# Optimization experiments

Hardware: AMD Instinct MI355X
Metric: run time of the kernel (lower is better)

Reference implementation:

```python
import jax, jax.numpy as jnp
import numpy as np

WINDOW = 128  # causal window width
D_SCALE = None  # set from val dim at trace time


def _softsign(x):
    return x / (1.0 + jnp.abs(x))


def setup_inputs() -> dict:
    key = jax.random.key(0)
    k1, k2 = jax.random.split(key)
    B, N, D = 4, 4096, 256
    val = jax.random.normal(k1, (B, N, D), dtype=jnp.float32)
    state = jax.random.normal(k2, (B, N), dtype=jnp.float32)
    return {"val": val, "state": state}


def reference(val, state):
    # val: [B, N, D], state: [B, N]
    B, N, D = val.shape
    # pairwise_fn: scaled dot product -> scores [B, N, N]
    scores = jnp.einsum('bnd,bmd->bnm', val, val) / jnp.sqrt(jnp.asarray(D, val.dtype))
    # edge_compress_fn: softsign
    edges = _softsign(scores)
    # causal window mask: source j satisfies (j <= i) & (j >= i - window)
    i = jnp.arange(N)[:, None]
    j = jnp.arange(N)[None, :]
    mask = (j <= i) & (j >= i - WINDOW)  # [N, N]
    edges = edges * mask[None, :, :].astype(edges.dtype)
    # val_proj_fn / state_proj_fn are Identity
    delta_state = jnp.einsum('bij,bj->bi', edges, state)   # [B, N]
    delta_val = jnp.einsum('bij,bjd->bid', edges, val)      # [B, N, D]
    return (delta_state, delta_val)
```

## Files before the change

### kernel.cpp

```cpp
#include <hip/hip_runtime.h>

#define NSEQ 4096
#define DIM  256
#define WIN  128
#define BATCH 4

typedef __bf16 bf16x8 __attribute__((ext_vector_type(8)));
typedef float  f32x4  __attribute__((ext_vector_type(4)));
typedef int    v2i    __attribute__((ext_vector_type(2)));
typedef int    v4i    __attribute__((ext_vector_type(4)));

__device__ __forceinline__ int sub_off(int j, int d) {
    return (((j >> 2) * 16 + (d >> 4)) << 6) + ((j & 3) << 4) + (d & 15);
}

__device__ __forceinline__ unsigned short f2bf(float f) {
    unsigned u = __builtin_bit_cast(unsigned, f);
    u += 0x7fffu + ((u >> 16) & 1u);
    return (unsigned short)(u >> 16);
}

__global__ __launch_bounds__(256, 2)
void sp_kernel(const float* __restrict__ val,
               const float* __restrict__ state,
               float* __restrict__ out) {
    __shared__ __align__(128) unsigned short vbuf[3][8192];
    __shared__ __align__(128) unsigned short E_s[2][32 * 56];
    __shared__ float ds_part[4][16];

    const int bx  = blockIdx.x;
    const int lbx = ((bx & 7) << 6) + (bx >> 3);
    const int b      = lbx >> 7;
    const int tile_i = lbx & 127;
    const int r0     = tile_i << 5;

    const int t   = threadIdx.x;
    const int w   = t >> 6;
    const int l   = t & 63;
    const int l15 = l & 15;
    const int l4  = l >> 4;
    const int mt  = w >> 1;
    const int jt  = w & 1;

    const float* valb = val + ((size_t)b * NSEQ) * DIM;
    const float* stb  = state + ((size_t)b * NSEQ);
    float* out_state  = out + ((size_t)b * NSEQ);
    float* out_val    = out + (size_t)BATCH * NSEQ + ((size_t)b * NSEQ) * DIM;

    const int s_jl[2] = {(w << 2) + l4, (w << 2) + l4 + 16};

    {
        const float* src = valb + ((size_t)tile_i << 13);
        #pragma unroll
        for (int p = 0; p < 8; ++p) {
            const int jl = s_jl[p & 1];
            const int d0 = (l15 << 2) + ((p >> 1) << 6);
            float4 v = *reinterpret_cast<const float4*>(src + jl * DIM + d0);
            ushort4 hh;
            hh.x = f2bf(v.x); hh.y = f2bf(v.y); hh.z = f2bf(v.z); hh.w = f2bf(v.w);
            *reinterpret_cast<ushort4*>(&vbuf[0][sub_off(jl, d0)]) = hh;
        }
    }
    __syncthreads();

    const int il = (mt << 4) + l15;
    const int jl = (jt << 4) + l15;
    bf16x8 af[8], sb[8];
    #pragma unroll
    for (int ks = 0; ks < 8; ++ks) {
        af[ks] = *reinterpret_cast<const bf16x8*>(&vbuf[0][sub_off(il, (l4 << 3) + (ks << 5))]);
        sb[ks] = *reinterpret_cast<const bf16x8*>(&vbuf[0][sub_off(jl, (l4 << 3) + (ks << 5))]);
    }

    const int tj0   = (tile_i >= 4) ? (tile_i - 4) : 0;
    const int ntile = tile_i - tj0 + 1;

    float dsacc[4] = {0.f, 0.f, 0.f, 0.f};
    f32x4 accpv[2][4];
    #pragma unroll
    for (int m2 = 0; m2 < 2; ++m2)
        #pragma unroll
        for (int tt = 0; tt < 4; ++tt)
            accpv[m2][tt] = (f32x4){0.f, 0.f, 0.f, 0.f};

    int bpi = 0;
    for (int q = 0; q < ntile; ++q) {
        const int ti = tile_i - q;
        const bool havenext = (q + 1 < ntile);
        const int bni = (bpi == 2) ? 0 : bpi + 1;
        const unsigned short* bp = &vbuf[bpi][0];
        unsigned short* bn = &vbuf[bni][0];
        unsigned short* Ecur = &E_s[q & 1][0];

        const int jg = (ti << 5) + jl;
        const float stv = stb[jg];
        float4 stg[8];
        if (havenext) {
            const float* src = valb + ((size_t)(ti - 1) << 13);
            #pragma unroll
            for (int qq = 0; qq < 8; ++qq)
                stg[qq] = *reinterpret_cast<const float4*>(src + s_jl[qq & 1] * DIM
                                                           + (l15 << 2) + ((qq >> 1) << 6));
        }

        f32x4 acc = (f32x4){0.f, 0.f, 0.f, 0.f};
        __builtin_amdgcn_s_setprio(1);
        #pragma unroll
        for (int ks = 0; ks < 8; ++ks)
            acc = __builtin_amdgcn_mfma_f32_16x16x32_bf16(af[ks], sb[ks], acc, 0, 0, 0);
        __builtin_amdgcn_s_setprio(0);

        const int ib = r0 + (mt << 4) + (l4 << 2);
        #pragma unroll
        for (int r = 0; r < 4; ++r) {
            float s = acc[r] * 0.0625f;
            float e = s / (1.0f + fabsf(s));
            const int ig = ib + r;
            if (jg > ig || jg < ig - WIN) e = 0.0f;
            dsacc[r] += e * stv;
            Ecur[((mt << 4) + (l4 << 2) + r) * 56 + (jt << 4) + l15] = f2bf(e);
        }

        if (havenext) {
            #pragma unroll
            for (int qq = 0; qq < 8; ++qq) {
                ushort4 hh;
                hh.x = f2bf(stg[qq].x); hh.y = f2bf(stg[qq].y);
                hh.z = f2bf(stg[qq].z); hh.w = f2bf(stg[qq].w);
                *reinterpret_cast<ushort4*>(&bn[sub_off(s_jl[qq & 1],
                                                        (l15 << 2) + ((qq >> 1) << 6))]) = hh;
            }
        }
        __syncthreads();

        bf16x8 ef0 = *reinterpret_cast<const bf16x8*>(&Ecur[l15 * 56 + (l4 << 3)]);
        bf16x8 ef1 = *reinterpret_cast<const bf16x8*>(&Ecur[(16 + l15) * 56 + (l4 << 3)]);
        if (havenext) {
            #pragma unroll
            for (int ks = 0; ks < 8; ++ks)
                sb[ks] = *reinterpret_cast<const bf16x8*>(&bn[sub_off(jl, (l4 << 3) + (ks << 5))]);
        }
        const unsigned lds_base = (unsigned)(size_t)bp;
        v2i tr[8];
        #pragma unroll
        for (int tt = 0; tt < 4; ++tt) {
            const int nt = (w << 2) + tt;
            unsigned a0 = lds_base + (unsigned)((((l4 << 5) + nt) << 7) + (l15 << 3));
            asm volatile("ds_read_b64_tr_b16 %0, %1" : "=v"(tr[2 * tt]) : "v"(a0) : "memory");
            asm volatile("ds_read_b64_tr_b16 %0, %1 offset:2048" : "=v"(tr[2 * tt + 1]) : "v"(a0) : "memory");
        }
        asm volatile("s_waitcnt lgkmcnt(0)" ::: "memory");
        __builtin_amdgcn_sched_barrier(0);
        __builtin_amdgcn_s_setprio(1);
        #pragma unroll
        for (int tt = 0; tt < 4; ++tt) {
            v4i tmp;
            tmp.x = tr[2 * tt].x; tmp.y = tr[2 * tt].y;
            tmp.z = tr[2 * tt + 1].x; tmp.w = tr[2 * tt + 1].y;
            bf16x8 bfr = __builtin_bit_cast(bf16x8, tmp);
            accpv[0][tt] = __builtin_amdgcn_mfma_f32_16x16x32_bf16(ef0, bfr, accpv[0][tt], 0, 0, 0);
            accpv[1][tt] = __builtin_amdgcn_mfma_f32_16x16x32_bf16(ef1, bfr, accpv[1][tt], 0, 0, 0);
        }
        __builtin_amdgcn_s_setprio(0);
        bpi = bni;
    }

    #pragma unroll
    for (int m = 1; m <= 8; m <<= 1) {
        #pragma unroll
        for (int r = 0; r < 4; ++r)
            dsacc[r] += __shfl_xor(dsacc[r], m, 64);
    }
    if (l15 == 0) {
        #pragma unroll
        for (int r = 0; r < 4; ++r)
            ds_part[w][(l4 << 2) + r] = dsacc[r];
    }
    __syncthreads();
    if (t < 32) {
        const int m2 = t >> 4;
        out_state[r0 + t] = ds_part[(m2 << 1)][t & 15] + ds_part[(m2 << 1) + 1][t & 15];
    }

    #pragma unroll
    for (int m2 = 0; m2 < 2; ++m2) {
        #pragma unroll
        for (int tt = 0; tt < 4; ++tt) {
            const int d = (w << 6) + (tt << 4) + l15;
            #pragma unroll
            for (int r = 0; r < 4; ++r) {
                const int ig = r0 + (m2 << 4) + (l4 << 2) + r;
                out_val[(size_t)ig * DIM + d] = accpv[m2][tt][r];
            }
        }
    }
}

extern "C" void kernel_launch(void* const* d_in, const int* in_sizes, int n_in,
                              void* d_out, int out_size, void* d_ws, size_t ws_size,
                              hipStream_t stream) {
    const float* val   = (const float*)d_in[0];
    const float* state = (const float*)d_in[1];
    float* out = (float*)d_out;
    sp_kernel<<<dim3(BATCH * (NSEQ / 32)), dim3(256), 0, stream>>>(val, state, out);
}
```

Measured before the change: 17.20 us.

## Prefetch global tiles two iterations ahead with packed bf16 conversion

Global loads of the val tiles now run two iterations ahead of use, alternating between two register staging arrays, and the first prefetch is issued alongside the initial tile load. The loop is fully unrolled to five iterations so buffer indices become compile-time constants. The float-to-bf16 conversion for staging uses the packed v_cvt_pk_bf16_f32 instruction, and the softsign divide is replaced by a hardware reciprocal. The aim is to hide global memory latency behind the MFMA work and cut conversion and divide ALU cost, in exchange for roughly 32 more VGPRs under a 2-waves-per-SIMD launch bound, which may cause spills.

Measured after the change: 16.98 us. About the same (-1.3%).

```diff
diff --git a/kernel.cpp b/kernel.cpp
--- a/kernel.cpp
+++ b/kernel.cpp
@@ -18,6 +18,34 @@
     unsigned u = __builtin_bit_cast(unsigned, f);
     u += 0x7fffu + ((u >> 16) & 1u);
     return (unsigned short)(u >> 16);
+}
+
+__device__ __forceinline__ unsigned pk2bf(float lo, float hi) {
+    unsigned r;
+    asm("v_cvt_pk_bf16_f32 %0, %1, %2" : "=v"(r) : "v"(lo), "v"(hi));
+    return r;
+}
+
+__device__ __forceinline__ void issue_loads(const float* __restrict__ src,
+                                            const int s_jl0, const int s_jl1,
+                                            const int l15, float4 (&dst)[8]) {
+    #pragma unroll
+    for (int qq = 0; qq < 8; ++qq)
+        dst[qq] = *reinterpret_cast<const float4*>(src + (qq & 1 ? s_jl1 : s_jl0) * DIM
+                                                   + (l15 << 2) + ((qq >> 1) << 6));
+}
+
+__device__ __forceinline__ void stage_write(unsigned short* __restrict__ bn,
+                                            const int s_jl0, const int s_jl1,
+                                            const int l15, const float4 (&stg)[8]) {
+    #pragma unroll
+    for (int qq = 0; qq < 8; ++qq) {
+        uint2 u;
+        u.x = pk2bf(stg[qq].x, stg[qq].y);
+        u.y = pk2bf(stg[qq].z, stg[qq].w);
+        *reinterpret_cast<uint2*>(&bn[sub_off(qq & 1 ? s_jl1 : s_jl0,
+                                              (l15 << 2) + ((qq >> 1) << 6))]) = u;
+    }
 }
 
 __global__ __launch_bounds__(256, 2)
@@ -47,19 +75,20 @@
     float* out_state  = out + ((size_t)b * NSEQ);
     float* out_val    = out + (size_t)BATCH * NSEQ + ((size_t)b * NSEQ) * DIM;
 
-    const int s_jl[2] = {(w << 2) + l4, (w << 2) + l4 + 16};
+    const int s_jl0 = (w << 2) + l4;
+    const int s_jl1 = s_jl0 + 16;
+
+    const int tj0   = (tile_i >= 4) ? (tile_i - 4) : 0;
+    const int ntile = tile_i - tj0 + 1;
+
+    float4 stgA[8], stgB[8];
 
     {
-        const float* src = valb + ((size_t)tile_i << 13);
-        #pragma unroll
-        for (int p = 0; p < 8; ++p) {
-            const int jl = s_jl[p & 1];
-            const int d0 = (l15 << 2) + ((p >> 1) << 6);
-            float4 v = *reinterpret_cast<const float4*>(src + jl * DIM + d0);
-            ushort4 hh;
-            hh.x = f2bf(v.x); hh.y = f2bf(v.y); hh.z = f2bf(v.z); hh.w = f2bf(v.w);
-            *reinterpret_cast<ushort4*>(&vbuf[0][sub_off(jl, d0)]) = hh;
-        }
+        float4 pv[8];
+        issue_loads(valb + ((size_t)tile_i << 13), s_jl0, s_jl1, l15, pv);
+        if (ntile > 1)
+            issue_loads(valb + ((size_t)(tile_i - 1) << 13), s_jl0, s_jl1, l15, stgB);
+        stage_write(&vbuf[0][0], s_jl0, s_jl1, l15, pv);
     }
     __syncthreads();
 
@@ -72,9 +101,6 @@
         sb[ks] = *reinterpret_cast<const bf16x8*>(&vbuf[0][sub_off(jl, (l4 << 3) + (ks << 5))]);
     }
 
-    const int tj0   = (tile_i >= 4) ? (tile_i - 4) : 0;
-    const int ntile = tile_i - tj0 + 1;
-
     float dsacc[4] = {0.f, 0.f, 0.f, 0.f};
     f32x4 accpv[2][4];
     #pragma unroll
@@ -83,24 +109,24 @@
         for (int tt = 0; tt < 4; ++tt)
             accpv[m2][tt] = (f32x4){0.f, 0.f, 0.f, 0.f};
 
-    int bpi = 0;
-    for (int q = 0; q < ntile; ++q) {
-        const int ti = tile_i - q;
-        const bool havenext = (q + 1 < ntile);
-        const int bni = (bpi == 2) ? 0 : bpi + 1;
-        const unsigned short* bp = &vbuf[bpi][0];
-        unsigned short* bn = &vbuf[bni][0];
+    #pragma unroll
+    for (int q = 0; q < 5; ++q) {
+        if (q >= ntile) break;
+        const int ti  = tile_i - q;
+        const int cs  = q % 3;
+        const int ns  = (q + 1) % 3;
+        const unsigned short* bp = &vbuf[cs][0];
+        unsigned short* bn = &vbuf[ns][0];
         unsigned short* Ecur = &E_s[q & 1][0];
 
         const int jg = (ti << 5) + jl;
         const float stv = stb[jg];
-        float4 stg[8];
-        if (havenext) {
-            const float* src = valb + ((size_t)(ti - 1) << 13);
-            #pragma unroll
-            for (int qq = 0; qq < 8; ++qq)
-                stg[qq] = *reinterpret_cast<const float4*>(src + s_jl[qq & 1] * DIM
-                                                           + (l15 << 2) + ((qq >> 1) << 6));
+
+        if (q + 2 < ntile) {
+            if ((q & 1) == 0)
+                issue_loads(valb + ((size_t)(ti - 2) << 13), s_jl0, s_jl1, l15, stgA);
+            else
+                issue_loads(valb + ((size_t)(ti - 2) << 13), s_jl0, s_jl1, l15, stgB);
         }
 
         f32x4 acc = (f32x4){0.f, 0.f, 0.f, 0.f};
@@ -114,28 +140,24 @@
         #pragma unroll
         for (int r = 0; r < 4; ++r) {
             float s = acc[r] * 0.0625f;
-            float e = s / (1.0f + fabsf(s));
+            float e = s * __builtin_amdgcn_rcpf(1.0f + fabsf(s));
             const int ig = ib + r;
             if (jg > ig || jg < ig - WIN) e = 0.0f;
             dsacc[r] += e * stv;
             Ecur[((mt << 4) + (l4 << 2) + r) * 56 + (jt << 4) + l15] = f2bf(e);
         }
 
-        if (havenext) {
-            #pragma unroll
-            for (int qq = 0; qq < 8; ++qq) {
-                ushort4 hh;
-                hh.x = f2bf(stg[qq].x); hh.y = f2bf(stg[qq].y);
-                hh.z = f2bf(stg[qq].z); hh.w = f2bf(stg[qq].w);
-                *reinterpret_cast<ushort4*>(&bn[sub_off(s_jl[qq & 1],
-                                                        (l15 << 2) + ((qq >> 1) << 6))]) = hh;
-            }
+        if (q + 1 < ntile) {
+            if ((q & 1) == 0)
+                stage_write(bn, s_jl0, s_jl1, l15, stgB);
+            else
+                stage_write(bn, s_jl0, s_jl1, l15, stgA);
         }
         __syncthreads();
 
         bf16x8 ef0 = *reinterpret_cast<const bf16x8*>(&Ecur[l15 * 56 + (l4 << 3)]);
         bf16x8 ef1 = *reinterpret_cast<const bf16x8*>(&Ecur[(16 + l15) * 56 + (l4 << 3)]);
-        if (havenext) {
+        if (q + 1 < ntile) {
             #pragma unroll
             for (int ks = 0; ks < 8; ++ks)
                 sb[ks] = *reinterpret_cast<const bf16x8*>(&bn[sub_off(jl, (l4 << 3) + (ks << 5))]);
@@ -155,14 +177,13 @@
         #pragma unroll
         for (int tt = 0; tt < 4; ++tt) {
             v4i tmp;
-            tmp.x = tr[2 * tt].x; tmp.y = tr[2 * tt].y;
+            tmp.x = tr[2 * tt].x;     tmp.y = tr[2 * tt].y;
             tmp.z = tr[2 * tt + 1].x; tmp.w = tr[2 * tt + 1].y;
             bf16x8 bfr = __builtin_bit_cast(bf16x8, tmp);
             accpv[0][tt] = __builtin_amdgcn_mfma_f32_16x16x32_bf16(ef0, bfr, accpv[0][tt], 0, 0, 0);
             accpv[1][tt] = __builtin_amdgcn_mfma_f32_16x16x32_bf16(ef1, bfr, accpv[1][tt], 0, 0, 0);
         }
         __builtin_amdgcn_s_setprio(0);
-        bpi = bni;
     }
 
     #pragma unroll
```

## Shrink LDS to double buffers and raise occupancy to four blocks per CU

Applied to the files above, without the earlier changes.

Cuts the val staging buffers from three to two and the edge buffer from two to one, and adds a second barrier per iteration so the buffers can be reused safely. Lowers LDS use and register pressure (sb is now loaded just before the QK MFMAs instead of prefetched) so launch bounds can ask for four blocks per CU. Also swaps the manual bf16 rounding for the packed v_cvt_pk_bf16_f32 instruction and the softsign division for a fast reciprocal. The extra barrier and the loss of the sb prefetch add per-iteration latency in exchange for more waves to hide it.

After: 47.44 us. 2.76x slower.

```diff
diff --git a/kernel.cpp b/kernel.cpp
--- a/kernel.cpp
+++ b/kernel.cpp
@@ -20,12 +20,18 @@
     return (unsigned short)(u >> 16);
 }
 
-__global__ __launch_bounds__(256, 2)
+__device__ __forceinline__ unsigned pk2bf(float lo, float hi) {
+    unsigned r;
+    asm("v_cvt_pk_bf16_f32 %0, %1, %2" : "=v"(r) : "v"(lo), "v"(hi));
+    return r;
+}
+
+__global__ __launch_bounds__(256, 4)
 void sp_kernel(const float* __restrict__ val,
                const float* __restrict__ state,
                float* __restrict__ out) {
-    __shared__ __align__(128) unsigned short vbuf[3][8192];
-    __shared__ __align__(128) unsigned short E_s[2][32 * 56];
+    __shared__ __align__(128) unsigned short vbuf[2][8192];
+    __shared__ __align__(128) unsigned short E_s[32 * 56];
     __shared__ float ds_part[4][16];
 
     const int bx  = blockIdx.x;
@@ -47,30 +53,30 @@
     float* out_state  = out + ((size_t)b * NSEQ);
     float* out_val    = out + (size_t)BATCH * NSEQ + ((size_t)b * NSEQ) * DIM;
 
-    const int s_jl[2] = {(w << 2) + l4, (w << 2) + l4 + 16};
+    const int s_jl0 = (w << 2) + l4;
+    const int s_jl1 = s_jl0 + 16;
 
     {
         const float* src = valb + ((size_t)tile_i << 13);
         #pragma unroll
-        for (int p = 0; p < 8; ++p) {
-            const int jl = s_jl[p & 1];
-            const int d0 = (l15 << 2) + ((p >> 1) << 6);
+        for (int qq = 0; qq < 8; ++qq) {
+            const int jl = (qq & 1) ? s_jl1 : s_jl0;
+            const int d0 = (l15 << 2) + ((qq >> 1) << 6);
             float4 v = *reinterpret_cast<const float4*>(src + jl * DIM + d0);
-            ushort4 hh;
-            hh.x = f2bf(v.x); hh.y = f2bf(v.y); hh.z = f2bf(v.z); hh.w = f2bf(v.w);
-            *reinterpret_cast<ushort4*>(&vbuf[0][sub_off(jl, d0)]) = hh;
+            uint2 u;
+            u.x = pk2bf(v.x, v.y);
+            u.y = pk2bf(v.z, v.w);
+            *reinterpret_cast<uint2*>(&vbuf[0][sub_off(jl, d0)]) = u;
         }
     }
     __syncthreads();
 
     const int il = (mt << 4) + l15;
     const int jl = (jt << 4) + l15;
-    bf16x8 af[8], sb[8];
-    #pragma unroll
-    for (int ks = 0; ks < 8; ++ks) {
+    bf16x8 af[8];
+    #pragma unroll
+    for (int ks = 0; ks < 8; ++ks)
         af[ks] = *reinterpret_cast<const bf16x8*>(&vbuf[0][sub_off(il, (l4 << 3) + (ks << 5))]);
-        sb[ks] = *reinterpret_cast<const bf16x8*>(&vbuf[0][sub_off(jl, (l4 << 3) + (ks << 5))]);
-    }
 
     const int tj0   = (tile_i >= 4) ? (tile_i - 4) : 0;
     const int ntile = tile_i - tj0 + 1;
@@ -83,26 +89,29 @@
         for (int tt = 0; tt < 4; ++tt)
             accpv[m2][tt] = (f32x4){0.f, 0.f, 0.f, 0.f};
 
-    int bpi = 0;
+    int p = 0;
     for (int q = 0; q < ntile; ++q) {
         const int ti = tile_i - q;
         const bool havenext = (q + 1 < ntile);
-        const int bni = (bpi == 2) ? 0 : bpi + 1;
-        const unsigned short* bp = &vbuf[bpi][0];
-        unsigned short* bn = &vbuf[bni][0];
-        unsigned short* Ecur = &E_s[q & 1][0];
+        const unsigned short* bp = &vbuf[p][0];
+        unsigned short* bn = &vbuf[1 - p][0];
 
         const int jg = (ti << 5) + jl;
         const float stv = stb[jg];
+
         float4 stg[8];
         if (havenext) {
             const float* src = valb + ((size_t)(ti - 1) << 13);
             #pragma unroll
             for (int qq = 0; qq < 8; ++qq)
-                stg[qq] = *reinterpret_cast<const float4*>(src + s_jl[qq & 1] * DIM
+                stg[qq] = *reinterpret_cast<const float4*>(src + ((qq & 1) ? s_jl1 : s_jl0) * DIM
                                                            + (l15 << 2) + ((qq >> 1) << 6));
         }
 
+        bf16x8 sb[8];
+        #pragma unroll
+        for (int ks = 0; ks < 8; ++ks)
+            sb[ks] = *reinterpret_cast<const bf16x8*>(&bp[sub_off(jl, (l4 << 3) + (ks << 5))]);
         f32x4 acc = (f32x4){0.f, 0.f, 0.f, 0.f};
         __builtin_amdgcn_s_setprio(1);
         #pragma unroll
@@ -114,32 +123,27 @@
         #pragma unroll
         for (int r = 0; r < 4; ++r) {
             float s = acc[r] * 0.0625f;
-            float e = s / (1.0f + fabsf(s));
+            float e = s * __builtin_amdgcn_rcpf(1.0f + fabsf(s));
             const int ig = ib + r;
             if (jg > ig || jg < ig - WIN) e = 0.0f;
             dsacc[r] += e * stv;
-            Ecur[((mt << 4) + (l4 << 2) + r) * 56 + (jt << 4) + l15] = f2bf(e);
+            E_s[((mt << 4) + (l4 << 2) + r) * 56 + (jt << 4) + l15] = f2bf(e);
         }
 
         if (havenext) {
             #pragma unroll
             for (int qq = 0; qq < 8; ++qq) {
-                ushort4 hh;
-                hh.x = f2bf(stg[qq].x); hh.y = f2bf(stg[qq].y);
-                hh.z = f2bf(stg[qq].z); hh.w = f2bf(stg[qq].w);
-                *reinterpret_cast<ushort4*>(&bn[sub_off(s_jl[qq & 1],
-                                                        (l15 << 2) + ((qq >> 1) << 6))]) = hh;
+                uint2 u;
+                u.x = pk2bf(stg[qq].x, stg[qq].y);
+                u.y = pk2bf(stg[qq].z, stg[qq].w);
+                *reinterpret_cast<uint2*>(&bn[sub_off((qq & 1) ? s_jl1 : s_jl0,
+                                                      (l15 << 2) + ((qq >> 1) << 6))]) = u;
             }
         }
         __syncthreads();
 
-        bf16x8 ef0 = *reinterpret_cast<const bf16x8*>(&Ecur[l15 * 56 + (l4 << 3)]);
-        bf16x8 ef1 = *reinterpret_cast<const bf16x8*>(&Ecur[(16 + l15) * 56 + (l4 << 3)]);
-        if (havenext) {
-            #pragma unroll
-            for (int ks = 0; ks < 8; ++ks)
-                sb[ks] = *reinterpret_cast<const bf16x8*>(&bn[sub_off(jl, (l4 << 3) + (ks << 5))]);
-        }
+        bf16x8 ef0 = *reinterpret_cast<const bf16x8*>(&E_s[l15 * 56 + (l4 << 3)]);
+        bf16x8 ef1 = *reinterpret_cast<const bf16x8*>(&E_s[(16 + l15) * 56 + (l4 << 3)]);
         const unsigned lds_base = (unsigned)(size_t)bp;
         v2i tr[8];
         #pragma unroll
@@ -155,14 +159,15 @@
         #pragma unroll
         for (int tt = 0; tt < 4; ++tt) {
             v4i tmp;
-            tmp.x = tr[2 * tt].x; tmp.y = tr[2 * tt].y;
+            tmp.x = tr[2 * tt].x;     tmp.y = tr[2 * tt].y;
             tmp.z = tr[2 * tt + 1].x; tmp.w = tr[2 * tt + 1].y;
             bf16x8 bfr = __builtin_bit_cast(bf16x8, tmp);
             accpv[0][tt] = __builtin_amdgcn_mfma_f32_16x16x32_bf16(ef0, bfr, accpv[0][tt], 0, 0, 0);
             accpv[1][tt] = __builtin_amdgcn_mfma_f32_16x16x32_bf16(ef1, bfr, accpv[1][tt], 0, 0, 0);
         }
         __builtin_amdgcn_s_setprio(0);
-        bpi = bni;
+        if (havenext) __syncthreads();
+        p ^= 1;
     }
 
     #pragma unroll
```
